# Optimization experiments

Hardware: AMD Instinct MI355X
Metric: run time of the kernel (lower is better)

## Reference

```python
import jax, jax.numpy as jnp
import numpy as np

DIM = 128
NUM_TILES = 50000
NUM_PIECES = 25000
E_TT = 600000
E_PT = 400000


def _mean_aggregate(msgs, dst, num_dst):
    # msgs: [E, dim], dst: [E] int -> [num_dst, dim]
    agg = jax.ops.segment_sum(msgs, dst, num_segments=num_dst)
    cnt = jax.ops.segment_sum(jnp.ones((dst.shape[0], 1), msgs.dtype), dst,
                              num_segments=num_dst)
    return agg / jnp.maximum(cnt, 1.0)


def _linear(x, W, b):
    # torch nn.Linear: y = x @ W.T + b, W: [out, in]
    return x @ W.T + b


def setup_inputs() -> dict:
    key = jax.random.key(0)
    ks = jax.random.split(key, 20)
    s = 1.0 / np.sqrt(DIM)
    s2 = 1.0 / np.sqrt(2 * DIM)
    inp = {
        "tile_h": jax.random.normal(ks[0], (NUM_TILES, DIM), jnp.float32),
        "piece_h": jax.random.normal(ks[1], (NUM_PIECES, DIM), jnp.float32),
        "tile_src": jax.random.randint(ks[2], (E_PT,), 0, NUM_TILES),
        "piece_dst": jax.random.randint(ks[3], (E_PT,), 0, NUM_PIECES),
        "piece_src": jax.random.randint(ks[4], (E_PT,), 0, NUM_PIECES),
        "tile_dst": jax.random.randint(ks[5], (E_PT,), 0, NUM_TILES),
        "t_src": jax.random.randint(ks[6], (E_TT,), 0, NUM_TILES),
        "t_dst": jax.random.randint(ks[7], (E_TT,), 0, NUM_TILES),
        # weights: torch Linear layout [out_features, in_features]
        "W_t2p": jax.random.uniform(ks[8], (DIM, DIM), jnp.float32, -s, s),
        "b_t2p": jax.random.uniform(ks[9], (DIM,), jnp.float32, -s, s),
        "W_pu": jax.random.uniform(ks[10], (DIM, 2 * DIM), jnp.float32, -s2, s2),
        "b_pu": jax.random.uniform(ks[11], (DIM,), jnp.float32, -s2, s2),
        "W_p2t": jax.random.uniform(ks[12], (DIM, DIM), jnp.float32, -s, s),
        "b_p2t": jax.random.uniform(ks[13], (DIM,), jnp.float32, -s, s),
        "W_tup": jax.random.uniform(ks[14], (DIM, 2 * DIM), jnp.float32, -s2, s2),
        "b_tup": jax.random.uniform(ks[15], (DIM,), jnp.float32, -s2, s2),
        "W_t2t": jax.random.uniform(ks[16], (DIM, DIM), jnp.float32, -s, s),
        "b_t2t": jax.random.uniform(ks[17], (DIM,), jnp.float32, -s, s),
        "W_tut": jax.random.uniform(ks[18], (DIM, 2 * DIM), jnp.float32, -s2, s2),
        "b_tut": jax.random.uniform(ks[19], (DIM,), jnp.float32, -s2, s2),
    }
    return inp


def reference(tile_h, piece_h, tile_src, piece_dst, piece_src, tile_dst,
              t_src, t_dst,
              W_t2p, b_t2p, W_pu, b_pu, W_p2t, b_p2t,
              W_tup, b_tup, W_t2t, b_t2t, W_tut, b_tut):
    num_tiles = tile_h.shape[0]
    num_pieces = piece_h.shape[0]

    # Stage 1: tile -> piece
    msgs = _linear(tile_h[tile_src], W_t2p, b_t2p)          # [E_pt, dim]
    agg = _mean_aggregate(msgs, piece_dst, num_pieces)
    piece_h = jax.nn.relu(_linear(jnp.concatenate([piece_h, agg], axis=1), W_pu, b_pu))

    # Stage 2: piece -> tile
    msgs = _linear(piece_h[piece_src], W_p2t, b_p2t)        # [E_pt, dim]
    agg = _mean_aggregate(msgs, tile_dst, num_tiles)
    tile_h = jax.nn.relu(_linear(jnp.concatenate([tile_h, agg], axis=1), W_tup, b_tup))

    # Stage 3: tile -> tile
    msgs = _linear(tile_h[t_src], W_t2t, b_t2t)             # [E_tt, dim]
    agg = _mean_aggregate(msgs, t_dst, num_tiles)
    tile_h = jax.nn.relu(_linear(jnp.concatenate([tile_h, agg], axis=1), W_tut, b_tut))

    return (tile_h, piece_h)
```

## Files before the change

kernel.cpp:

```cpp
#include <hip/hip_runtime.h>
#include <hip/hip_bf16.h>

#define DIM 128

typedef unsigned short u16;
typedef unsigned int u32;
typedef __attribute__((ext_vector_type(8))) short v8s;
typedef __attribute__((ext_vector_type(4))) float v4f;

__device__ __forceinline__ float bf2f(u16 u) {
    union { unsigned int i; float f; } v;
    v.i = ((unsigned int)u) << 16;
    return v.f;
}

__device__ __forceinline__ u16 f2bf(float f) {
    union { float f; unsigned int i; } v;
    v.f = f;
    unsigned int x = v.i;
    return (u16)((x + 0x7fffu + ((x >> 16) & 1u)) >> 16);
}

__device__ __forceinline__ uint4 pack8(float4 x0, float4 x1) {
    uint4 o;
    o.x = (u32)f2bf(x0.x) | ((u32)f2bf(x0.y) << 16);
    o.y = (u32)f2bf(x0.z) | ((u32)f2bf(x0.w) << 16);
    o.z = (u32)f2bf(x1.x) | ((u32)f2bf(x1.y) << 16);
    o.w = (u32)f2bf(x1.z) | ((u32)f2bf(x1.w) << 16);
    return o;
}

struct CvtArgs { const float* s[8]; u32 pfx[9]; };
__global__ __launch_bounds__(256) void cvt_all(CvtArgs a, u16* __restrict__ dst, int n8)
{
    int g = blockIdx.x * 256 + threadIdx.x;
    if (g >= n8) return;
    u32 flat = (u32)g * 8;
    int seg = 0;
    #pragma unroll
    for (int i = 1; i < 8; ++i) if (flat >= a.pfx[i]) seg = i;
    const float4* fp = (const float4*)(a.s[seg] + (flat - a.pfx[seg]));
    *(uint4*)(dst + flat) = pack8(fp[0], fp[1]);
}

__global__ __launch_bounds__(256) void zeroi_kernel(int* __restrict__ p, int n)
{
    int i = blockIdx.x * 256 + threadIdx.x;
    if (i < n) p[i] = 0;
}

__global__ __launch_bounds__(256) void hist3(
    const int* __restrict__ piece_dst, const int* __restrict__ tile_dst,
    const int* __restrict__ t_dst, int EPT, int ETT,
    int* __restrict__ deg, int* __restrict__ epos, int NP, int NT)
{
    int e = blockIdx.x * 256 + threadIdx.x;
    int pos;
    if (e < EPT)                 pos = atomicAdd(&deg[piece_dst[e]], 1);
    else if (e < 2 * EPT)        pos = atomicAdd(&deg[NP + tile_dst[e - EPT]], 1);
    else if (e < 2 * EPT + ETT)  pos = atomicAdd(&deg[NP + NT + t_dst[e - 2 * EPT]], 1);
    else return;
    epos[e] = pos;
}

__global__ __launch_bounds__(256) void scan_part3(const int* __restrict__ deg,
                                                  int* __restrict__ partial,
                                                  int* __restrict__ bsum,
                                                  int NP, int NT)
{
    const int B1 = (NP + 2047) >> 11, B2 = (NT + 2047) >> 11;
    int b = blockIdx.x, lb, Nseg, base, bsb;
    if (b < B1)           { lb = b;            Nseg = NP; base = 0;       bsb = 0;  }
    else if (b < B1 + B2) { lb = b - B1;       Nseg = NT; base = NP;      bsb = 16; }
    else                  { lb = b - B1 - B2;  Nseg = NT; base = NP + NT; bsb = 64; }

    __shared__ int ls[256];
    const int lbase = lb * 2048;
    const int t = threadIdx.x;
    int v[8];
    int s = 0;
    #pragma unroll
    for (int i = 0; i < 8; ++i) {
        int idx = lbase + t * 8 + i;
        v[i] = (idx < Nseg) ? deg[base + idx] : 0;
        s += v[i];
    }
    ls[t] = s;
    __syncthreads();
    #pragma unroll
    for (int o = 1; o < 256; o <<= 1) {
        int x = (t >= o) ? ls[t - o] : 0;
        __syncthreads();
        ls[t] += x;
        __syncthreads();
    }
    int run = (t == 0) ? 0 : ls[t - 1];
    #pragma unroll
    for (int i = 0; i < 8; ++i) {
        int idx = lbase + t * 8 + i;
        if (idx < Nseg) partial[base + idx] = run;
        run += v[i];
    }
    if (t == 255) bsum[bsb + lb] = ls[255];
}

__global__ __launch_bounds__(256) void scan_fix3(const int* __restrict__ partial,
                                                 const int* __restrict__ bsum,
                                                 int* __restrict__ rowptr,
                                                 int NP, int NT, int EPT, int ETT)
{
    const int B1 = (NP + 2047) >> 11, B2 = (NT + 2047) >> 11;
    int b = blockIdx.x, lb, Nseg, base, bsb, rb, Eseg;
    if (b < B1)           { lb = b;           Nseg = NP; base = 0;       bsb = 0;  rb = 0;                  Eseg = EPT; }
    else if (b < B1 + B2) { lb = b - B1;      Nseg = NT; base = NP;      bsb = 16; rb = NP + 1;             Eseg = EPT; }
    else                  { lb = b - B1 - B2; Nseg = NT; base = NP + NT; bsb = 64; rb = NP + 1 + NT + 1;    Eseg = ETT; }

    __shared__ int off_s;
    const int t = threadIdx.x;
    if (t == 0) {
        int o = 0;
        for (int i = 0; i < lb; ++i) o += bsum[bsb + i];
        off_s = o;
    }
    __syncthreads();
    const int off = off_s;
    const int lbase = lb * 2048;
    #pragma unroll
    for (int i = 0; i < 8; ++i) {
        int idx = lbase + t * 8 + i;
        if (idx < Nseg) rowptr[rb + idx] = partial[base + idx] + off;
    }
    int lastlb = ((Nseg + 2047) >> 11) - 1;
    if (lb == lastlb && t == 255) rowptr[rb + Nseg] = Eseg;
}

__global__ __launch_bounds__(256) void fill_direct(
    const int* __restrict__ tile_src, const int* __restrict__ piece_dst,
    const int* __restrict__ piece_src, const int* __restrict__ tile_dst,
    const int* __restrict__ t_src, const int* __restrict__ t_dst,
    int EPT, int ETT,
    const int* __restrict__ rowptr, const int* __restrict__ epos,
    int* __restrict__ el, int NP, int NT)
{
    int e = blockIdx.x * 256 + threadIdx.x;
    int d, s, segOff;
    const int* rp;
    if (e < EPT) {
        d = piece_dst[e]; s = tile_src[e];
        rp = rowptr; segOff = 0;
    } else if (e < 2 * EPT) {
        int le = e - EPT;
        d = tile_dst[le]; s = piece_src[le];
        rp = rowptr + NP + 1; segOff = EPT;
    } else if (e < 2 * EPT + ETT) {
        int le = e - 2 * EPT;
        d = t_dst[le]; s = t_src[le];
        rp = rowptr + NP + 1 + NT + 1; segOff = 2 * EPT;
    } else return;
    el[segOff + rp[d] + epos[e]] = s;
}

__global__ __launch_bounds__(256) void gather_mean_kernel(
    const u16* __restrict__ feat,
    const int* __restrict__ elist, const int* __restrict__ rowptr,
    int N, u16* __restrict__ meanA)
{
    int node = blockIdx.x * 8 + (threadIdx.x >> 5);
    int lane = threadIdx.x & 31;
    if (node >= N) return;
    int r0 = rowptr[node], r1 = rowptr[node + 1];
    float a0 = 0.f, a1 = 0.f, a2 = 0.f, a3 = 0.f;
    float b0 = 0.f, b1 = 0.f, b2 = 0.f, b3 = 0.f;
    int j = r0;
    for (; j + 4 <= r1; j += 4) {
        int s0 = elist[j], s1 = elist[j + 1], s2 = elist[j + 2], s3 = elist[j + 3];
        uint2 v0 = ((const uint2*)(feat + (size_t)s0 * DIM))[lane];
        uint2 v1 = ((const uint2*)(feat + (size_t)s1 * DIM))[lane];
        uint2 v2 = ((const uint2*)(feat + (size_t)s2 * DIM))[lane];
        uint2 v3 = ((const uint2*)(feat + (size_t)s3 * DIM))[lane];
        a0 += bf2f((u16)(v0.x & 0xffffu)); a1 += bf2f((u16)(v0.x >> 16));
        a2 += bf2f((u16)(v0.y & 0xffffu)); a3 += bf2f((u16)(v0.y >> 16));
        b0 += bf2f((u16)(v1.x & 0xffffu)); b1 += bf2f((u16)(v1.x >> 16));
        b2 += bf2f((u16)(v1.y & 0xffffu)); b3 += bf2f((u16)(v1.y >> 16));
        a0 += bf2f((u16)(v2.x & 0xffffu)); a1 += bf2f((u16)(v2.x >> 16));
        a2 += bf2f((u16)(v2.y & 0xffffu)); a3 += bf2f((u16)(v2.y >> 16));
        b0 += bf2f((u16)(v3.x & 0xffffu)); b1 += bf2f((u16)(v3.x >> 16));
        b2 += bf2f((u16)(v3.y & 0xffffu)); b3 += bf2f((u16)(v3.y >> 16));
    }
    for (; j < r1; ++j) {
        int s = elist[j];
        uint2 v = ((const uint2*)(feat + (size_t)s * DIM))[lane];
        a0 += bf2f((u16)(v.x & 0xffffu)); a1 += bf2f((u16)(v.x >> 16));
        a2 += bf2f((u16)(v.y & 0xffffu)); a3 += bf2f((u16)(v.y >> 16));
    }
    a0 += b0; a1 += b1; a2 += b2; a3 += b3;
    float sc = (r1 > r0) ? (1.f / (float)(r1 - r0)) : 0.f;
    uint2 o;
    o.x = (u32)f2bf(a0 * sc) | ((u32)f2bf(a1 * sc) << 16);
    o.y = (u32)f2bf(a2 * sc) | ((u32)f2bf(a3 * sc) << 16);
    ((uint2*)(meanA + (size_t)node * DIM))[lane] = o;
}

__global__ __launch_bounds__(256) void stage_fused(
    const u16* __restrict__ meanA, const int* __restrict__ rowptr,
    const u16* __restrict__ Wt, const float* __restrict__ bt,
    const u16* __restrict__ A1, const u16* __restrict__ Wu,
    const float* __restrict__ bu,
    u16* __restrict__ outC, float* __restrict__ outF, int N)
{
    __shared__ u16 Wl[128][136];
    __shared__ u16 Al[64][136];
    __shared__ u16 Bl[64][136];
    const int tid = threadIdx.x;
    const int nb = blockIdx.x * 64;
    const int wave = tid >> 6;
    const int lane = tid & 63;
    const int m = lane & 15;
    const int quad = lane >> 4;
    const int arow = wave * 16 + m;

    #pragma unroll
    for (int i = 0; i < 8; ++i) {
        int c = i * 256 + tid;
        int row = c >> 4;
        int c8 = (c & 15) * 8;
        *(uint4*)&Wl[row][c8] = *(const uint4*)(Wt + row * 128 + c8);
    }
    #pragma unroll
    for (int i = 0; i < 4; ++i) {
        int c = i * 256 + tid;
        int row = c >> 4;
        int c8 = (c & 15) * 8;
        int n = nb + row;
        uint4 v = {0u, 0u, 0u, 0u};
        if (n < N) v = *(const uint4*)(meanA + (size_t)n * DIM + c8);
        *(uint4*)&Al[row][c8] = v;
    }
    __syncthreads();

    v4f acct[8];
    #pragma unroll
    for (int t = 0; t < 8; ++t) acct[t] = (v4f){0.f, 0.f, 0.f, 0.f};
    #pragma unroll
    for (int k0 = 0; k0 < 128; k0 += 32) {
        v8s a = *(const v8s*)&Al[arow][k0 + quad * 8];
        #pragma unroll
        for (int t = 0; t < 8; ++t) {
            v8s b = *(const v8s*)&Wl[t * 16 + m][k0 + quad * 8];
            acct[t] = __builtin_amdgcn_mfma_f32_16x16x32_bf16(a, b, acct[t], 0, 0, 0);
        }
    }
    __syncthreads();

    {
        float btv[8];
        #pragma unroll
        for (int t = 0; t < 8; ++t) btv[t] = bt[t * 16 + m];
        #pragma unroll
        for (int r = 0; r < 4; ++r) {
            int n = nb + wave * 16 + quad * 4 + r;
            bool has = (n < N) && (rowptr[n + 1] > rowptr[n]);
            #pragma unroll
            for (int t = 0; t < 8; ++t) {
                float val = has ? (acct[t][r] + btv[t]) : 0.f;
                Bl[wave * 16 + quad * 4 + r][t * 16 + m] = f2bf(val);
            }
        }
    }
    #pragma unroll
    for (int i = 0; i < 8; ++i) {
        int c = i * 256 + tid;
        int row = c >> 4;
        int c8 = (c & 15) * 8;
        *(uint4*)&Wl[row][c8] = *(const uint4*)(Wu + row * 256 + c8);
    }
    #pragma unroll
    for (int i = 0; i < 4; ++i) {
        int c = i * 256 + tid;
        int row = c >> 4;
        int c8 = (c & 15) * 8;
        int n = nb + row;
        uint4 v = {0u, 0u, 0u, 0u};
        if (n < N) v = *(const uint4*)(A1 + (size_t)n * DIM + c8);
        *(uint4*)&Al[row][c8] = v;
    }
    __syncthreads();

    v4f accu[8];
    #pragma unroll
    for (int t = 0; t < 8; ++t) accu[t] = (v4f){0.f, 0.f, 0.f, 0.f};
    #pragma unroll
    for (int k0 = 0; k0 < 128; k0 += 32) {
        v8s a = *(const v8s*)&Al[arow][k0 + quad * 8];
        #pragma unroll
        for (int t = 0; t < 8; ++t) {
            v8s b = *(const v8s*)&Wl[t * 16 + m][k0 + quad * 8];
            accu[t] = __builtin_amdgcn_mfma_f32_16x16x32_bf16(a, b, accu[t], 0, 0, 0);
        }
    }
    __syncthreads();

    #pragma unroll
    for (int i = 0; i < 8; ++i) {
        int c = i * 256 + tid;
        int row = c >> 4;
        int c8 = (c & 15) * 8;
        *(uint4*)&Wl[row][c8] = *(const uint4*)(Wu + row * 256 + 128 + c8);
    }
    __syncthreads();

    #pragma unroll
    for (int k0 = 0; k0 < 128; k0 += 32) {
        v8s a = *(const v8s*)&Bl[arow][k0 + quad * 8];
        #pragma unroll
        for (int t = 0; t < 8; ++t) {
            v8s b = *(const v8s*)&Wl[t * 16 + m][k0 + quad * 8];
            accu[t] = __builtin_amdgcn_mfma_f32_16x16x32_bf16(a, b, accu[t], 0, 0, 0);
        }
    }

    float buv[8];
    #pragma unroll
    for (int t = 0; t < 8; ++t) buv[t] = bu[t * 16 + m];
    #pragma unroll
    for (int r = 0; r < 4; ++r) {
        int n = nb + wave * 16 + quad * 4 + r;
        if (n >= N) continue;
        #pragma unroll
        for (int t = 0; t < 8; ++t) {
            float val = accu[t][r] + buv[t];
            val = val > 0.f ? val : 0.f;
            if (outC) outC[(size_t)n * DIM + t * 16 + m] = f2bf(val);
            if (outF) outF[(size_t)n * DIM + t * 16 + m] = val;
        }
    }
}

extern "C" void kernel_launch(void* const* d_in, const int* in_sizes, int n_in,
                              void* d_out, int out_size, void* d_ws, size_t ws_size,
                              hipStream_t stream)
{
    const float* tile_h   = (const float*)d_in[0];
    const float* piece_h  = (const float*)d_in[1];
    const int* tile_src   = (const int*)d_in[2];
    const int* piece_dst  = (const int*)d_in[3];
    const int* piece_src  = (const int*)d_in[4];
    const int* tile_dst   = (const int*)d_in[5];
    const int* t_src      = (const int*)d_in[6];
    const int* t_dst      = (const int*)d_in[7];
    const float* b_t2p = (const float*)d_in[9];
    const float* b_pu  = (const float*)d_in[11];
    const float* b_p2t = (const float*)d_in[13];
    const float* b_tup = (const float*)d_in[15];
    const float* b_t2t = (const float*)d_in[17];
    const float* b_tut = (const float*)d_in[19];

    const int NT  = in_sizes[0] / DIM;
    const int NP  = in_sizes[1] / DIM;
    const int EPT = in_sizes[2];
    const int ETT = in_sizes[6];
    const int ET  = 2 * EPT + ETT;

    char* ws = (char*)d_ws;
    size_t off = 0;
    int* deg = (int*)(ws + off);      off += (size_t)(NP + 2 * NT) * sizeof(int);
    off = (off + 255) & ~(size_t)255;
    int* partial = (int*)(ws + off);  off += (size_t)(NP + 2 * NT) * sizeof(int);
    off = (off + 255) & ~(size_t)255;
    int* rowptr = (int*)(ws + off);   off += (size_t)(NP + 2 * NT + 3) * sizeof(int);
    off = (off + 255) & ~(size_t)255;
    int* bsum = (int*)(ws + off);     off += 128 * sizeof(int);
    off = (off + 255) & ~(size_t)255;
    int* el = (int*)(ws + off);       off += (size_t)ET * sizeof(int);
    off = (off + 255) & ~(size_t)255;
    u16* A = (u16*)(ws + off);        off += (size_t)NT * DIM * sizeof(u16);
    off = (off + 255) & ~(size_t)255;
    u16* C = (u16*)(ws + off);        off += (size_t)NT * DIM * sizeof(u16);
    off = (off + 255) & ~(size_t)255;
    u16* arena = (u16*)(ws + off);

    int* epos = (int*)A;

    const u32 nTh = (u32)NT * DIM, nPh = (u32)NP * DIM;
    u32 pfx[9];
    pfx[0] = 0;
    pfx[1] = nTh;
    pfx[2] = pfx[1] + nPh;
    pfx[3] = pfx[2] + 16384;
    pfx[4] = pfx[3] + 32768;
    pfx[5] = pfx[4] + 16384;
    pfx[6] = pfx[5] + 32768;
    pfx[7] = pfx[6] + 16384;
    pfx[8] = pfx[7] + 32768;

    u16* Th = arena + pfx[0];
    u16* Ph = arena + pfx[1];
    const u16* Wt2p = arena + pfx[2];
    const u16* Wpu  = arena + pfx[3];
    const u16* Wp2t = arena + pfx[4];
    const u16* Wtup = arena + pfx[5];
    const u16* Wt2t = arena + pfx[6];
    const u16* Wtut = arena + pfx[7];

    int* rp1 = rowptr;
    int* rp2 = rowptr + NP + 1;
    int* rp3 = rowptr + NP + 1 + NT + 1;
    int* el1 = el;
    int* el2 = el + EPT;
    int* el3 = el + 2 * EPT;

    float* out_tile  = (float*)d_out;
    float* out_piece = out_tile + (size_t)NT * DIM;

    dim3 blk(256);
    const int B1 = (NP + 2047) >> 11, B2 = (NT + 2047) >> 11;
    dim3 g_scan((unsigned)(B1 + 2 * B2));
    dim3 g_edges((unsigned)((ET + 255) / 256));
    dim3 g_zdeg((unsigned)((NP + 2 * NT + 255) / 256));
    dim3 g_gp((unsigned)((NP + 7) / 8));
    dim3 g_gt((unsigned)((NT + 7) / 8));
    dim3 g_np((unsigned)((NP + 63) / 64));
    dim3 g_nt((unsigned)((NT + 63) / 64));

    CvtArgs ca;
    ca.s[0] = tile_h; ca.s[1] = piece_h;
    ca.s[2] = (const float*)d_in[8];  ca.s[3] = (const float*)d_in[10];
    ca.s[4] = (const float*)d_in[12]; ca.s[5] = (const float*)d_in[14];
    ca.s[6] = (const float*)d_in[16]; ca.s[7] = (const float*)d_in[18];
    for (int i = 0; i < 9; ++i) ca.pfx[i] = pfx[i];
    int n8 = (int)(pfx[8] / 8);
    hipLaunchKernelGGL(cvt_all, dim3((n8 + 255) / 256), blk, 0, stream, ca, arena, n8);

    hipLaunchKernelGGL(zeroi_kernel, g_zdeg, blk, 0, stream, deg, NP + 2 * NT);
    hipLaunchKernelGGL(hist3, g_edges, blk, 0, stream,
                       piece_dst, tile_dst, t_dst, EPT, ETT, deg, epos, NP, NT);
    hipLaunchKernelGGL(scan_part3, g_scan, blk, 0, stream, deg, partial, bsum, NP, NT);
    hipLaunchKernelGGL(scan_fix3, g_scan, blk, 0, stream,
                       partial, bsum, rowptr, NP, NT, EPT, ETT);
    hipLaunchKernelGGL(fill_direct, g_edges, blk, 0, stream,
                       tile_src, piece_dst, piece_src, tile_dst, t_src, t_dst,
                       EPT, ETT, rowptr, epos, el, NP, NT);

    hipLaunchKernelGGL(gather_mean_kernel, g_gp, blk, 0, stream,
                       Th, el1, rp1, NP, A);
    hipLaunchKernelGGL(stage_fused, g_np, blk, 0, stream,
                       A, rp1, Wt2p, b_t2p, Ph, Wpu, b_pu, C, out_piece, NP);

    hipLaunchKernelGGL(gather_mean_kernel, g_gt, blk, 0, stream,
                       C, el2, rp2, NT, A);
    hipLaunchKernelGGL(stage_fused, g_nt, blk, 0, stream,
                       A, rp2, Wp2t, b_p2t, Th, Wtup, b_tup, C, (float*)nullptr, NT);

    hipLaunchKernelGGL(gather_mean_kernel, g_gt, blk, 0, stream,
                       C, el3, rp3, NT, A);
    hipLaunchKernelGGL(stage_fused, g_nt, blk, 0, stream,
                       A, rp3, Wt2t, b_t2t, C, Wtut, b_tut, (u16*)nullptr, out_tile, NT);
}
```

Before: 339.3 us.

## Build CSR via two-pass bucketed radix sort instead of global atomics

Replaces the global-atomic degree histogram plus direct fill with a two-level radix partition. Edges are first scattered into 512 coarse buckets using per-block shared-memory histograms and a global scan. Each bucket is then sorted in shared memory, which emits both rowptr and the edge lists. This removes contended global atomics and random scatter writes, and groups edges of nearby destinations together. The cost is an extra pass over the edges, and the packed 17-bit source field limits node counts.

```diff
diff --git a/kernel.cpp b/kernel.cpp
--- a/kernel.cpp
+++ b/kernel.cpp
@@ -2,6 +2,8 @@
 #include <hip/hip_bf16.h>
 
 #define DIM 128
+#define EPB 4096
+#define BINS 512
 
 typedef unsigned short u16;
 typedef unsigned int u32;
@@ -43,46 +45,44 @@
     *(uint4*)(dst + flat) = pack8(fp[0], fp[1]);
 }
 
-__global__ __launch_bounds__(256) void zeroi_kernel(int* __restrict__ p, int n)
-{
-    int i = blockIdx.x * 256 + threadIdx.x;
-    if (i < n) p[i] = 0;
-}
-
-__global__ __launch_bounds__(256) void hist3(
+__global__ __launch_bounds__(256) void rs_count(
     const int* __restrict__ piece_dst, const int* __restrict__ tile_dst,
     const int* __restrict__ t_dst, int EPT, int ETT,
-    int* __restrict__ deg, int* __restrict__ epos, int NP, int NT)
-{
-    int e = blockIdx.x * 256 + threadIdx.x;
-    int pos;
-    if (e < EPT)                 pos = atomicAdd(&deg[piece_dst[e]], 1);
-    else if (e < 2 * EPT)        pos = atomicAdd(&deg[NP + tile_dst[e - EPT]], 1);
-    else if (e < 2 * EPT + ETT)  pos = atomicAdd(&deg[NP + NT + t_dst[e - 2 * EPT]], 1);
-    else return;
-    epos[e] = pos;
-}
-
-__global__ __launch_bounds__(256) void scan_part3(const int* __restrict__ deg,
-                                                  int* __restrict__ partial,
-                                                  int* __restrict__ bsum,
-                                                  int NP, int NT)
-{
-    const int B1 = (NP + 2047) >> 11, B2 = (NT + 2047) >> 11;
-    int b = blockIdx.x, lb, Nseg, base, bsb;
-    if (b < B1)           { lb = b;            Nseg = NP; base = 0;       bsb = 0;  }
-    else if (b < B1 + B2) { lb = b - B1;       Nseg = NT; base = NP;      bsb = 16; }
-    else                  { lb = b - B1 - B2;  Nseg = NT; base = NP + NT; bsb = 64; }
-
+    int* __restrict__ counts, int NBLK)
+{
+    __shared__ int h[BINS];
+    const int t = threadIdx.x;
+    for (int d = t; d < BINS; d += 256) h[d] = 0;
+    __syncthreads();
+    const int blk = blockIdx.x;
+    const int ET = 2 * EPT + ETT;
+    #pragma unroll
+    for (int j = 0; j < EPB / 256; ++j) {
+        int e = blk * EPB + j * 256 + t;
+        if (e < ET) {
+            int d;
+            if (e < EPT)            d = (piece_dst[e] >> 9);
+            else if (e < 2 * EPT)   d = 128 | (tile_dst[e - EPT] >> 9);
+            else                    d = 256 | (t_dst[e - 2 * EPT] >> 9);
+            atomicAdd(&h[d], 1);
+        }
+    }
+    __syncthreads();
+    for (int d = t; d < BINS; d += 256) counts[d * NBLK + blk] = h[d];
+}
+
+__global__ __launch_bounds__(256) void scan_gpart(const int* __restrict__ in,
+                                                  int* __restrict__ out,
+                                                  int* __restrict__ bsum, int n)
+{
     __shared__ int ls[256];
-    const int lbase = lb * 2048;
-    const int t = threadIdx.x;
-    int v[8];
-    int s = 0;
+    const int blk = blockIdx.x, t = threadIdx.x;
+    const int base = blk * 2048;
+    int v[8]; int s = 0;
     #pragma unroll
     for (int i = 0; i < 8; ++i) {
-        int idx = lbase + t * 8 + i;
-        v[i] = (idx < Nseg) ? deg[base + idx] : 0;
+        int idx = base + t * 8 + i;
+        v[i] = (idx < n) ? in[idx] : 0;
         s += v[i];
     }
     ls[t] = s;
@@ -97,67 +97,117 @@
     int run = (t == 0) ? 0 : ls[t - 1];
     #pragma unroll
     for (int i = 0; i < 8; ++i) {
-        int idx = lbase + t * 8 + i;
-        if (idx < Nseg) partial[base + idx] = run;
+        int idx = base + t * 8 + i;
+        if (idx < n) out[idx] = run;
         run += v[i];
     }
-    if (t == 255) bsum[bsb + lb] = ls[255];
-}
-
-__global__ __launch_bounds__(256) void scan_fix3(const int* __restrict__ partial,
-                                                 const int* __restrict__ bsum,
-                                                 int* __restrict__ rowptr,
-                                                 int NP, int NT, int EPT, int ETT)
-{
-    const int B1 = (NP + 2047) >> 11, B2 = (NT + 2047) >> 11;
-    int b = blockIdx.x, lb, Nseg, base, bsb, rb, Eseg;
-    if (b < B1)           { lb = b;           Nseg = NP; base = 0;       bsb = 0;  rb = 0;                  Eseg = EPT; }
-    else if (b < B1 + B2) { lb = b - B1;      Nseg = NT; base = NP;      bsb = 16; rb = NP + 1;             Eseg = EPT; }
-    else                  { lb = b - B1 - B2; Nseg = NT; base = NP + NT; bsb = 64; rb = NP + 1 + NT + 1;    Eseg = ETT; }
-
+    if (t == 255) bsum[blk] = ls[255];
+}
+
+__global__ __launch_bounds__(256) void scan_gfix(int* __restrict__ out,
+                                                 const int* __restrict__ bsum, int n)
+{
     __shared__ int off_s;
-    const int t = threadIdx.x;
+    const int blk = blockIdx.x, t = threadIdx.x;
     if (t == 0) {
         int o = 0;
-        for (int i = 0; i < lb; ++i) o += bsum[bsb + i];
+        for (int i = 0; i < blk; ++i) o += bsum[i];
         off_s = o;
     }
     __syncthreads();
     const int off = off_s;
-    const int lbase = lb * 2048;
+    const int base = blk * 2048;
     #pragma unroll
     for (int i = 0; i < 8; ++i) {
-        int idx = lbase + t * 8 + i;
-        if (idx < Nseg) rowptr[rb + idx] = partial[base + idx] + off;
-    }
-    int lastlb = ((Nseg + 2047) >> 11) - 1;
-    if (lb == lastlb && t == 255) rowptr[rb + Nseg] = Eseg;
-}
-
-__global__ __launch_bounds__(256) void fill_direct(
+        int idx = base + t * 8 + i;
+        if (idx < n) out[idx] += off;
+    }
+}
+
+__global__ __launch_bounds__(256) void rs_scatter(
     const int* __restrict__ tile_src, const int* __restrict__ piece_dst,
     const int* __restrict__ piece_src, const int* __restrict__ tile_dst,
     const int* __restrict__ t_src, const int* __restrict__ t_dst,
     int EPT, int ETT,
-    const int* __restrict__ rowptr, const int* __restrict__ epos,
-    int* __restrict__ el, int NP, int NT)
-{
-    int e = blockIdx.x * 256 + threadIdx.x;
-    int d, s, segOff;
-    const int* rp;
-    if (e < EPT) {
-        d = piece_dst[e]; s = tile_src[e];
-        rp = rowptr; segOff = 0;
-    } else if (e < 2 * EPT) {
-        int le = e - EPT;
-        d = tile_dst[le]; s = piece_src[le];
-        rp = rowptr + NP + 1; segOff = EPT;
-    } else if (e < 2 * EPT + ETT) {
-        int le = e - 2 * EPT;
-        d = t_dst[le]; s = t_src[le];
-        rp = rowptr + NP + 1 + NT + 1; segOff = 2 * EPT;
-    } else return;
-    el[segOff + rp[d] + epos[e]] = s;
+    const int* __restrict__ countsS, int NBLK, int* __restrict__ T)
+{
+    __shared__ int p[BINS];
+    const int t = threadIdx.x;
+    const int blk = blockIdx.x;
+    for (int d = t; d < BINS; d += 256) p[d] = countsS[d * NBLK + blk];
+    __syncthreads();
+    const int ET = 2 * EPT + ETT;
+    #pragma unroll
+    for (int j = 0; j < EPB / 256; ++j) {
+        int e = blk * EPB + j * 256 + t;
+        if (e < ET) {
+            int dst, src, d;
+            if (e < EPT) {
+                dst = piece_dst[e]; src = tile_src[e]; d = dst >> 9;
+            } else if (e < 2 * EPT) {
+                int le = e - EPT;
+                dst = tile_dst[le]; src = piece_src[le]; d = 128 | (dst >> 9);
+            } else {
+                int le = e - 2 * EPT;
+                dst = t_dst[le]; src = t_src[le]; d = 256 | (dst >> 9);
+            }
+            int pos = atomicAdd(&p[d], 1);
+            T[pos] = ((dst & 511) << 17) | src;
+        }
+    }
+}
+
+__global__ __launch_bounds__(256) void bucket_sort(
+    const int* __restrict__ T, const int* __restrict__ countsS, int NBLK, int ET,
+    int EPT, int ETT, int NP, int NT,
+    int* __restrict__ el, int* __restrict__ rowptr)
+{
+    const int d = blockIdx.x;
+    const int seg = d >> 7;
+    if (seg > 2) return;
+    const int dhi = d & 127;
+    int Nseg, segOff, rb, Eseg;
+    if (seg == 0)      { Nseg = NP; segOff = 0;       rb = 0;                 Eseg = EPT; }
+    else if (seg == 1) { Nseg = NT; segOff = EPT;     rb = NP + 1;            Eseg = EPT; }
+    else               { Nseg = NT; segOff = 2 * EPT; rb = NP + 1 + NT + 1;   Eseg = ETT; }
+
+    const int bstart = countsS[d * NBLK];
+    const int bend = (d < BINS - 1) ? countsS[(d + 1) * NBLK] : ET;
+
+    __shared__ int hist[BINS];
+    __shared__ int pos[BINS];
+    __shared__ int ls[256];
+    const int t = threadIdx.x;
+    for (int i = t; i < BINS; i += 256) hist[i] = 0;
+    __syncthreads();
+    for (int j = bstart + t; j < bend; j += 256)
+        atomicAdd(&hist[T[j] >> 17], 1);
+    __syncthreads();
+    int c0 = hist[2 * t], c1 = hist[2 * t + 1];
+    ls[t] = c0 + c1;
+    __syncthreads();
+    #pragma unroll
+    for (int o = 1; o < 256; o <<= 1) {
+        int x = (t >= o) ? ls[t - o] : 0;
+        __syncthreads();
+        ls[t] += x;
+        __syncthreads();
+    }
+    int ex = (t == 0) ? 0 : ls[t - 1];
+    pos[2 * t]     = bstart + ex;
+    pos[2 * t + 1] = bstart + ex + c0;
+    __syncthreads();
+    for (int i = t; i < BINS; i += 256) {
+        int n = dhi * 512 + i;
+        if (n < Nseg) rowptr[rb + n] = pos[i] - segOff;
+    }
+    if (t == 0 && dhi == ((Nseg - 1) >> 9)) rowptr[rb + Nseg] = Eseg;
+    __syncthreads();
+    for (int j = bstart + t; j < bend; j += 256) {
+        int v = T[j];
+        int p = atomicAdd(&pos[v >> 17], 1);
+        el[p] = v & 0x1ffff;
+    }
 }
 
 __global__ __launch_bounds__(256) void gather_mean_kernel(
@@ -361,16 +411,20 @@
     const int ETT = in_sizes[6];
     const int ET  = 2 * EPT + ETT;
 
+    const int NBLK = (ET + EPB - 1) / EPB;
+    const int n2 = BINS * NBLK;
+    const int SB = (n2 + 2047) / 2048;
+
     char* ws = (char*)d_ws;
     size_t off = 0;
-    int* deg = (int*)(ws + off);      off += (size_t)(NP + 2 * NT) * sizeof(int);
-    off = (off + 255) & ~(size_t)255;
-    int* partial = (int*)(ws + off);  off += (size_t)(NP + 2 * NT) * sizeof(int);
+    int* counts = (int*)(ws + off);   off += (size_t)n2 * sizeof(int);
+    off = (off + 255) & ~(size_t)255;
+    int* countsS = (int*)(ws + off);  off += (size_t)n2 * sizeof(int);
+    off = (off + 255) & ~(size_t)255;
+    int* gbsum = (int*)(ws + off);    off += (size_t)((SB + 63) & ~63) * sizeof(int);
     off = (off + 255) & ~(size_t)255;
     int* rowptr = (int*)(ws + off);   off += (size_t)(NP + 2 * NT + 3) * sizeof(int);
     off = (off + 255) & ~(size_t)255;
-    int* bsum = (int*)(ws + off);     off += 128 * sizeof(int);
-    off = (off + 255) & ~(size_t)255;
     int* el = (int*)(ws + off);       off += (size_t)ET * sizeof(int);
     off = (off + 255) & ~(size_t)255;
     u16* A = (u16*)(ws + off);        off += (size_t)NT * DIM * sizeof(u16);
@@ -379,7 +433,7 @@
     off = (off + 255) & ~(size_t)255;
     u16* arena = (u16*)(ws + off);
 
-    int* epos = (int*)A;
+    int* T = (int*)A;
 
     const u32 nTh = (u32)NT * DIM, nPh = (u32)NP * DIM;
     u32 pfx[9];
@@ -413,10 +467,9 @@
     float* out_piece = out_tile + (size_t)NT * DIM;
 
     dim3 blk(256);
-    const int B1 = (NP + 2047) >> 11, B2 = (NT + 2047) >> 11;
-    dim3 g_scan((unsigned)(B1 + 2 * B2));
-    dim3 g_edges((unsigned)((ET + 255) / 256));
-    dim3 g_zdeg((unsigned)((NP + 2 * NT + 255) / 256));
+    dim3 g_rs((unsigned)NBLK);
+    dim3 g_scan((unsigned)SB);
+    dim3 g_bs((unsigned)BINS);
     dim3 g_gp((unsigned)((NP + 7) / 8));
     dim3 g_gt((unsigned)((NT + 7) / 8));
     dim3 g_np((unsigned)((NP + 63) / 64));
@@ -431,15 +484,15 @@
     int n8 = (int)(pfx[8] / 8);
     hipLaunchKernelGGL(cvt_all, dim3((n8 + 255) / 256), blk, 0, stream, ca, arena, n8);
 
-    hipLaunchKernelGGL(zeroi_kernel, g_zdeg, blk, 0, stream, deg, NP + 2 * NT);
-    hipLaunchKernelGGL(hist3, g_edges, blk, 0, stream,
-                       piece_dst, tile_dst, t_dst, EPT, ETT, deg, epos, NP, NT);
-    hipLaunchKernelGGL(scan_part3, g_scan, blk, 0, stream, deg, partial, bsum, NP, NT);
-    hipLaunchKernelGGL(scan_fix3, g_scan, blk, 0, stream,
-                       partial, bsum, rowptr, NP, NT, EPT, ETT);
-    hipLaunchKernelGGL(fill_direct, g_edges, blk, 0, stream,
+    hipLaunchKernelGGL(rs_count, g_rs, blk, 0, stream,
+                       piece_dst, tile_dst, t_dst, EPT, ETT, counts, NBLK);
+    hipLaunchKernelGGL(scan_gpart, g_scan, blk, 0, stream, counts, countsS, gbsum, n2);
+    hipLaunchKernelGGL(scan_gfix, g_scan, blk, 0, stream, countsS, gbsum, n2);
+    hipLaunchKernelGGL(rs_scatter, g_rs, blk, 0, stream,
                        tile_src, piece_dst, piece_src, tile_dst, t_src, t_dst,
-                       EPT, ETT, rowptr, epos, el, NP, NT);
+                       EPT, ETT, countsS, NBLK, T);
+    hipLaunchKernelGGL(bucket_sort, g_bs, blk, 0, stream,
+                       T, countsS, NBLK, ET, EPT, ETT, NP, NT, el, rowptr);
 
     hipLaunchKernelGGL(gather_mean_kernel, g_gp, blk, 0, stream,
                        Th, el1, rp1, NP, A);
```

After: 312.1 us. -8.0%, faster.
